# Performance work log

Measured on AMD Instinct MI355X. Metric: run time of the kernel, lower is better.

Reference implementation:

```python
import jax, jax.numpy as jnp
import numpy as np

D_MODEL = 768
D_COND = 128
N_LAYERS = 6
D_STATE = 16
D_CONV = 4
EXPAND = 2
D_INNER = EXPAND * D_MODEL            # 1536
DT_RANK = (D_MODEL + 15) // 16        # 48
BATCH, SEQ = 2, 1024
EPS = 1e-5


def setup_inputs() -> dict:
    key = jax.random.key(0)
    ks = iter(jax.random.split(key, 24))
    rn = lambda shape, s=0.02: jax.random.normal(next(ks), shape, dtype=jnp.float32) * s
    inp = {}
    inp["x"] = jax.random.normal(next(ks), (BATCH, SEQ, D_MODEL), dtype=jnp.float32)
    inp["condition"] = jax.random.normal(next(ks), (BATCH, D_COND), dtype=jnp.float32)
    # per-layer Mamba params, stacked on leading layer dim
    inp["in_proj_w"] = rn((N_LAYERS, 2 * D_INNER, D_MODEL))
    inp["conv_w"] = rn((N_LAYERS, D_INNER, D_CONV), 0.1)
    inp["conv_b"] = jnp.zeros((N_LAYERS, D_INNER), jnp.float32)
    inp["x_proj_w"] = rn((N_LAYERS, DT_RANK + 2 * D_STATE, D_INNER))
    inp["dt_proj_w"] = rn((N_LAYERS, D_INNER, DT_RANK), 0.1)
    inp["dt_proj_b"] = jnp.full((N_LAYERS, D_INNER), -4.0, jnp.float32)  # softplus -> small dt
    inp["A_log"] = jnp.tile(jnp.log(jnp.arange(1, D_STATE + 1, dtype=jnp.float32))[None, None, :], (N_LAYERS, D_INNER, 1))
    inp["D_skip"] = jnp.ones((N_LAYERS, D_INNER), jnp.float32)
    inp["out_proj_w"] = rn((N_LAYERS, D_MODEL, D_INNER))
    # post-residual LayerNorm affine per layer
    inp["norm_w"] = jnp.ones((N_LAYERS, D_MODEL), jnp.float32)
    inp["norm_b"] = jnp.zeros((N_LAYERS, D_MODEL), jnp.float32)
    # AdaLN: condition -> (scale, shift)
    inp["adaln_w"] = rn((N_LAYERS, 2 * D_MODEL, D_COND))
    inp["adaln_b"] = jnp.zeros((N_LAYERS, 2 * D_MODEL), jnp.float32)
    inp["final_norm_w"] = jnp.ones((D_MODEL,), jnp.float32)
    inp["final_norm_b"] = jnp.zeros((D_MODEL,), jnp.float32)
    return inp


def _ln(h, w, b):
    mu = jnp.mean(h, -1, keepdims=True)
    var = jnp.mean(jnp.square(h - mu), -1, keepdims=True)
    return (h - mu) * jax.lax.rsqrt(var + EPS) * w + b


def _ln_noaffine(h):
    mu = jnp.mean(h, -1, keepdims=True)
    var = jnp.mean(jnp.square(h - mu), -1, keepdims=True)
    return (h - mu) * jax.lax.rsqrt(var + EPS)


def _mamba(x, in_w, cw, cb, xp_w, dtp_w, dtp_b, A_log, D_skip, out_w):
    b, l, _ = x.shape
    xz = jnp.einsum('bld,ed->ble', x, in_w)                 # [b,l,2*di]
    xc, z = jnp.split(xz, 2, axis=-1)
    # causal depthwise conv over time
    xc_t = jnp.transpose(xc, (0, 2, 1))                     # [b,di,l]
    xc_t = jax.lax.conv_general_dilated(
        xc_t, cw[:, None, :], window_strides=(1,), padding=[(D_CONV - 1, 0)],
        dimension_numbers=('NCH', 'OIH', 'NCH'), feature_group_count=D_INNER)
    xc = jnp.transpose(xc_t + cb[None, :, None], (0, 2, 1))  # [b,l,di]
    xc = jax.nn.silu(xc)
    dbc = jnp.einsum('bld,ed->ble', xc, xp_w)                # [b,l,dt_rank+2*ds]
    dt = dbc[..., :DT_RANK]
    Bm = dbc[..., DT_RANK:DT_RANK + D_STATE]                 # [b,l,ds]
    Cm = dbc[..., DT_RANK + D_STATE:]                        # [b,l,ds]
    dt = jax.nn.softplus(jnp.einsum('blr,dr->bld', dt, dtp_w) + dtp_b)  # [b,l,di]
    A = -jnp.exp(A_log)                                      # [di,ds]

    def step(h, ts):
        dt_t, B_t, C_t, x_t = ts                             # [b,di],[b,ds],[b,ds],[b,di]
        dA = jnp.exp(dt_t[:, :, None] * A)                   # [b,di,ds]
        h = dA * h + (dt_t * x_t)[:, :, None] * B_t[:, None, :]
        y = jnp.sum(h * C_t[:, None, :], axis=-1)            # [b,di]
        return h, y

    h0 = jnp.zeros((b, D_INNER, D_STATE), x.dtype)
    ts = (jnp.transpose(dt, (1, 0, 2)), jnp.transpose(Bm, (1, 0, 2)),
          jnp.transpose(Cm, (1, 0, 2)), jnp.transpose(xc, (1, 0, 2)))
    h_final, y = jax.lax.scan(step, h0, ts)
    y = jnp.transpose(y, (1, 0, 2)) + D_skip * xc            # [b,l,di]
    y = y * jax.nn.silu(z)
    out = jnp.einsum('bld,ed->ble', y, out_w)                # [b,l,dm]
    return out, h_final


def reference(x, condition, in_proj_w, conv_w, conv_b, x_proj_w, dt_proj_w, dt_proj_b,
              A_log, D_skip, out_proj_w, norm_w, norm_b, adaln_w, adaln_b,
              final_norm_w, final_norm_b):
    h = x
    states = []
    for i in range(N_LAYERS):
        residual = h
        m, st = _mamba(h, in_proj_w[i], conv_w[i], conv_b[i], x_proj_w[i],
                       dt_proj_w[i], dt_proj_b[i], A_log[i], D_skip[i], out_proj_w[i])
        h = _ln(residual + m, norm_w[i], norm_b[i])
        ss = condition @ adaln_w[i].T + adaln_b[i]            # [b,2*dm]
        scale, shift = jnp.split(ss, 2, axis=-1)
        h = _ln_noaffine(h) * (1.0 + scale[:, None, :]) + shift[:, None, :]
        states.append(st)
    h = _ln(h, final_norm_w, final_norm_b)
    return h, jnp.stack(states)
```

## Files before the change

kernel.cpp:

```cpp
#include <hip/hip_runtime.h>
#include <hip/hip_bf16.h>

#define NL 6
#define DM 768
#define DI 1536
#define DS 16
#define NRANK 48
#define DBC 80
#define BATCH 2
#define SEQ 1024
#define NTOK (BATCH*SEQ)
#define NCHUNK 64
#define CHLEN 16
#define XKS 8
#define XKC (DI/XKS)

typedef __attribute__((ext_vector_type(8))) short short8;
typedef __attribute__((ext_vector_type(8))) unsigned short ushort8v;
typedef __attribute__((ext_vector_type(4))) float f32x4;
typedef __attribute__((ext_vector_type(4))) unsigned short ushort4v;

__device__ inline unsigned short f2bf(float f) {
  union { float f; unsigned u; } x; x.f = f;
  unsigned r = x.u + 0x7FFF + ((x.u >> 16) & 1);
  return (unsigned short)(r >> 16);
}
__device__ inline float bf2f(unsigned short s) {
  union { unsigned u; float f; } x; x.u = ((unsigned)s) << 16;
  return x.f;
}

__device__ inline void gl_lds16(const unsigned short* g, unsigned short* l) {
  __builtin_amdgcn_global_load_lds(
      (const __attribute__((address_space(1))) unsigned int*)(g),
      (__attribute__((address_space(3))) unsigned int*)(l),
      16, 0, 0);
}

#define V_X   (NTOK * DM / 8)
#define V_INW (NL * 2 * DI * DM / 8)
#define V_OUW (NL * DM * DI / 8)
#define V_XPW (NL * DBC * DI / 8)
#define V_DTW (NL * DI * 64 / 8)
#define V_NA  (NL * DI * DS / 8)
#define V_DTA (NTOK * 64 / 8)
#define V_ADA (NL * BATCH * 2 * DM)

__device__ inline ushort8v cvt8v(f32x4 a, f32x4 b) {
  union { ushort8v u8; __hip_bfloat162 h[4]; } u;
  float2 p;
  p.x = a[0]; p.y = a[1]; u.h[0] = __float22bfloat162_rn(p);
  p.x = a[2]; p.y = a[3]; u.h[1] = __float22bfloat162_rn(p);
  p.x = b[0]; p.y = b[1]; u.h[2] = __float22bfloat162_rn(p);
  p.x = b[2]; p.y = b[3]; u.h[3] = __float22bfloat162_rn(p);
  return u.u8;
}
__device__ inline void cvt8_store(const float* s, unsigned short* d, int i) {
  f32x4 a = ((const f32x4*)s)[i * 2];
  f32x4 b = ((const f32x4*)s)[i * 2 + 1];
  ((ushort8v*)d)[i] = cvt8v(a, b);
}

__global__ __launch_bounds__(256) void cvt_k(
    const float* __restrict__ x, const float* __restrict__ inw,
    const float* __restrict__ ouw, const float* __restrict__ xpw,
    const float* __restrict__ dtpw, const float* __restrict__ alog,
    const float* __restrict__ cond, const float* __restrict__ adaw,
    const float* __restrict__ adab,
    unsigned short* __restrict__ xb, unsigned short* __restrict__ inwb,
    unsigned short* __restrict__ ouwb, unsigned short* __restrict__ xpwb,
    unsigned short* __restrict__ dtwb, float* __restrict__ na,
    unsigned short* __restrict__ dtA, float* __restrict__ ss) {
  const int gid = blockIdx.x * 256 + threadIdx.x;
  const int stride = gridDim.x * 256;
  for (int i = gid; i < V_X; i += stride) cvt8_store(x, xb, i);
  for (int i = gid; i < V_INW; i += stride) cvt8_store(inw, inwb, i);
  for (int i = gid; i < V_OUW; i += stride) cvt8_store(ouw, ouwb, i);
  for (int i = gid; i < V_XPW; i += stride) cvt8_store(xpw, xpwb, i);
  for (int i = gid; i < V_DTW; i += stride) {
    int col8 = (i & 7) * 8;
    int row = i >> 3;
    ushort8v u8;
    if (col8 < NRANK) {
      const float* src = dtpw + (size_t)row * NRANK + col8;
      f32x4 a = *(const f32x4*)src;
      f32x4 b = *(const f32x4*)(src + 4);
      u8 = cvt8v(a, b);
    } else {
      u8 = (ushort8v){0,0,0,0,0,0,0,0};
    }
    *(ushort8v*)&dtwb[(size_t)row * 64 + col8] = u8;
  }
  for (int i = gid; i < V_NA; i += stride) {
    f32x4 a = ((const f32x4*)alog)[i * 2];
    f32x4 b = ((const f32x4*)alog)[i * 2 + 1];
    f32x4 ra, rb;
#pragma unroll
    for (int e = 0; e < 4; e++) { ra[e] = -__expf(a[e]); rb[e] = -__expf(b[e]); }
    ((f32x4*)na)[i * 2] = ra;
    ((f32x4*)na)[i * 2 + 1] = rb;
  }
  for (int i = gid; i < V_DTA; i += stride)
    ((ushort8v*)dtA)[i] = (ushort8v){0,0,0,0,0,0,0,0};
  for (int i = gid; i < V_ADA; i += stride) {
    int e = i % (2 * DM);
    int b = (i / (2 * DM)) % BATCH;
    int l = i / (BATCH * 2 * DM);
    const float* c = cond + b * 128;
    const float* wp = adaw + ((size_t)l * (2 * DM) + e) * 128;
    float s = adab[l * (2 * DM) + e];
    for (int kk = 0; kk < 128; kk++) s = fmaf(c[kk], wp[kk], s);
    ss[i] = s;
  }
}

__global__ __launch_bounds__(256) void bt128b_k(
    const unsigned short* __restrict__ A, int lda,
    const unsigned short* __restrict__ W, int ldw,
    unsigned short* __restrict__ C, int ldc,
    int K) {
  __shared__ __align__(16) unsigned short As[3][128 * 32];
  __shared__ __align__(16) unsigned short Ws[3][128 * 32];
  const int tid = threadIdx.x;
  const int bm = blockIdx.y * 128;
  const int bn = blockIdx.x * 128;
  const int lane = tid & 63;
  const int wv = tid >> 6;
  const int wm = (wv >> 1) * 64;
  const int wn = (wv & 1) * 64;
  const int fr = lane & 15;
  const int fs = lane >> 4;

  const int r0 = tid >> 2;
  const int s0 = (tid & 3) ^ (r0 & 3);

  const unsigned short* gA0 = A + (size_t)(bm + r0) * lda + s0 * 8;
  const unsigned short* gA1 = A + (size_t)(bm + r0 + 64) * lda + s0 * 8;
  const unsigned short* gW0 = W + (size_t)(bn + r0) * ldw + s0 * 8;
  const unsigned short* gW1 = W + (size_t)(bn + r0 + 64) * ldw + s0 * 8;

  f32x4 acc[4][4];
#pragma unroll
  for (int i = 0; i < 4; i++)
#pragma unroll
    for (int j = 0; j < 4; j++) acc[i][j] = (f32x4){0.f, 0.f, 0.f, 0.f};

  const int nk = K >> 5;
  gl_lds16(gA0, &As[0][0] + tid * 8);
  gl_lds16(gA1, &As[0][2048] + tid * 8);
  gl_lds16(gW0, &Ws[0][0] + tid * 8);
  gl_lds16(gW1, &Ws[0][2048] + tid * 8);
  if (nk > 1) {
    gl_lds16(gA0 + 32, &As[1][0] + tid * 8);
    gl_lds16(gA1 + 32, &As[1][2048] + tid * 8);
    gl_lds16(gW0 + 32, &Ws[1][0] + tid * 8);
    gl_lds16(gW1 + 32, &Ws[1][2048] + tid * 8);
  }

  for (int kk = 0; kk < nk; kk++) {
    const int b = kk % 3;
    if (kk + 2 < nk) {
      const int k0 = (kk + 2) * 32;
      const int nb = (kk + 2) % 3;
      gl_lds16(gA0 + k0, &As[nb][0] + tid * 8);
      gl_lds16(gA1 + k0, &As[nb][2048] + tid * 8);
      gl_lds16(gW0 + k0, &Ws[nb][0] + tid * 8);
      gl_lds16(gW1 + k0, &Ws[nb][2048] + tid * 8);
    }
    const int ahead = (nk - 1 - kk >= 2) ? 2 : (nk - 1 - kk);
    if (ahead == 2)      asm volatile("s_waitcnt vmcnt(8)" : : : "memory");
    else if (ahead == 1) asm volatile("s_waitcnt vmcnt(4)" : : : "memory");
    else                 asm volatile("s_waitcnt vmcnt(0)" : : : "memory");
    __builtin_amdgcn_s_barrier();
    __builtin_amdgcn_sched_barrier(0);

    short8 af[4], bf[4];
#pragma unroll
    for (int i = 0; i < 4; i++) {
      int rowa = wm + i * 16 + fr;
      af[i] = *(const short8*)&As[b][rowa * 32 + ((fs ^ (rowa & 3)) * 8)];
      int rowb = wn + i * 16 + fr;
      bf[i] = *(const short8*)&Ws[b][rowb * 32 + ((fs ^ (rowb & 3)) * 8)];
    }
#pragma unroll
    for (int i = 0; i < 4; i++)
#pragma unroll
      for (int j = 0; j < 4; j++)
        acc[i][j] = __builtin_amdgcn_mfma_f32_16x16x32_bf16(af[i], bf[j], acc[i][j], 0, 0, 0);

    __builtin_amdgcn_s_barrier();
  }

#pragma unroll
  for (int i = 0; i < 4; i++) {
#pragma unroll
    for (int j = 0; j < 4; j++) {
#pragma unroll
      for (int r = 0; r < 4; r++) {
        int row = bm + wm + i * 16 + fs * 4 + r;
        int col = bn + wn + j * 16 + fr;
        C[(size_t)row * ldc + col] = f2bf(acc[i][j][r]);
      }
    }
  }
}

template<int EPI>
__global__ __launch_bounds__(256) void bt64_k(
    const unsigned short* __restrict__ A, int lda,
    const unsigned short* __restrict__ W, int ldw,
    void* __restrict__ Cv, int ldc,
    int K,
    const float* __restrict__ bias) {
  __shared__ __align__(16) unsigned short As[3][64 * 32];
  __shared__ __align__(16) unsigned short Ws[3][64 * 32];
  const int tid = threadIdx.x;
  const int bm = blockIdx.y * 64;
  const int bn = blockIdx.x * 64;
  const int kz = (EPI == 3) ? blockIdx.z : 0;
  const int lane = tid & 63;
  const int wv = tid >> 6;
  const int wm = (wv >> 1) * 32;
  const int wn = (wv & 1) * 32;
  const int fr = lane & 15;
  const int fs = lane >> 4;

  const int r0 = tid >> 2;
  const int s0 = (tid & 3) ^ (r0 & 3);

  const unsigned short* gA = A + (size_t)(bm + r0) * lda + kz * K + s0 * 8;
  const unsigned short* gW = W + (size_t)(bn + r0) * ldw + kz * K + s0 * 8;

  f32x4 acc[2][2];
#pragma unroll
  for (int i = 0; i < 2; i++)
#pragma unroll
    for (int j = 0; j < 2; j++) acc[i][j] = (f32x4){0.f, 0.f, 0.f, 0.f};

  const int nk = K >> 5;
  gl_lds16(gA, &As[0][0] + tid * 8);
  gl_lds16(gW, &Ws[0][0] + tid * 8);
  if (nk > 1) {
    gl_lds16(gA + 32, &As[1][0] + tid * 8);
    gl_lds16(gW + 32, &Ws[1][0] + tid * 8);
  }

  for (int kk = 0; kk < nk; kk++) {
    const int b = kk % 3;
    if (kk + 2 < nk) {
      const int k0 = (kk + 2) * 32;
      const int nb = (kk + 2) % 3;
      gl_lds16(gA + k0, &As[nb][0] + tid * 8);
      gl_lds16(gW + k0, &Ws[nb][0] + tid * 8);
    }
    const int ahead = (nk - 1 - kk >= 2) ? 2 : (nk - 1 - kk);
    if (ahead == 2)      asm volatile("s_waitcnt vmcnt(4)" : : : "memory");
    else if (ahead == 1) asm volatile("s_waitcnt vmcnt(2)" : : : "memory");
    else                 asm volatile("s_waitcnt vmcnt(0)" : : : "memory");
    __builtin_amdgcn_s_barrier();
    __builtin_amdgcn_sched_barrier(0);

    short8 af[2], bf[2];
#pragma unroll
    for (int i = 0; i < 2; i++) {
      int rowa = wm + i * 16 + fr;
      af[i] = *(const short8*)&As[b][rowa * 32 + ((fs ^ (rowa & 3)) * 8)];
      int rowb = wn + i * 16 + fr;
      bf[i] = *(const short8*)&Ws[b][rowb * 32 + ((fs ^ (rowb & 3)) * 8)];
    }
#pragma unroll
    for (int i = 0; i < 2; i++)
#pragma unroll
      for (int j = 0; j < 2; j++)
        acc[i][j] = __builtin_amdgcn_mfma_f32_16x16x32_bf16(af[i], bf[j], acc[i][j], 0, 0, 0);

    __builtin_amdgcn_s_barrier();
  }

#pragma unroll
  for (int i = 0; i < 2; i++) {
#pragma unroll
    for (int j = 0; j < 2; j++) {
#pragma unroll
      for (int r = 0; r < 4; r++) {
        int row = bm + wm + i * 16 + fs * 4 + r;
        int col = bn + wn + j * 16 + fr;
        float v = acc[i][j][r];
        if (EPI == 1) {
          float xv = v + bias[col];
          float sp = (xv > 20.f) ? xv : log1pf(__expf(xv));
          ((unsigned short*)Cv)[(size_t)row * ldc + col] = f2bf(sp);
        }
        if (EPI == 3) {
          ((float*)Cv)[((size_t)kz * NTOK + row) * ldc + col] = v;
        }
      }
    }
  }
}

__global__ __launch_bounds__(256) void xp_k(
    const unsigned short* __restrict__ A,
    const unsigned short* __restrict__ W,
    unsigned short* __restrict__ part) {
  __shared__ __align__(16) unsigned short As[64][40];
  __shared__ __align__(16) unsigned short Ws[80][40];
  const int tid = threadIdx.x;
  const int ks = blockIdx.x;
  const int bm = blockIdx.y * 64;
  const int lane = tid & 63;
  const int wv = tid >> 6;
  const int fr = lane & 15;
  const int fs = lane >> 4;
  const int fk = fs * 8;

  const int ar = tid >> 2;
  const int ac = (tid & 3) * 8;
  const int k0base = ks * XKC;

  const unsigned short* gA  = A + (size_t)(bm + ar) * DI + k0base + ac;
  const unsigned short* gW0 = W + (size_t)ar * DI + k0base + ac;
  const unsigned short* gW1 = W + (size_t)(64 + ar) * DI + k0base + ac;

  f32x4 acc[5];
#pragma unroll
  for (int n = 0; n < 5; n++) acc[n] = (f32x4){0.f, 0.f, 0.f, 0.f};

  short8 aA, w0A, w1A;
  aA = *(const short8*)(gA);
  w0A = *(const short8*)(gW0);
  if (tid < 64) w1A = *(const short8*)(gW1);

  const int nk = XKC / 32;
  for (int kk = 0; kk < nk; kk++) {
    __syncthreads();
    *(short8*)&As[ar][ac] = aA;
    *(short8*)&Ws[ar][ac] = w0A;
    if (tid < 64) *(short8*)&Ws[64 + ar][ac] = w1A;
    __syncthreads();

    if (kk + 1 < nk) {
      const int k0 = (kk + 1) * 32;
      aA = *(const short8*)(gA + k0);
      w0A = *(const short8*)(gW0 + k0);
      if (tid < 64) w1A = *(const short8*)(gW1 + k0);
    }

    short8 af = *(const short8*)&As[wv * 16 + fr][fk];
#pragma unroll
    for (int n = 0; n < 5; n++) {
      short8 bf = *(const short8*)&Ws[n * 16 + fr][fk];
      acc[n] = __builtin_amdgcn_mfma_f32_16x16x32_bf16(af, bf, acc[n], 0, 0, 0);
    }
  }

#pragma unroll
  for (int n = 0; n < 5; n++) {
#pragma unroll
    for (int r = 0; r < 4; r++) {
      int row = bm + wv * 16 + fs * 4 + r;
      part[((size_t)ks * NTOK + row) * DBC + n * 16 + fr] = f2bf(acc[n][r]);
    }
  }
}

__global__ __launch_bounds__(256) void xp_reduce_k(const unsigned short* __restrict__ part,
                                                   unsigned short* __restrict__ dtA,
                                                   unsigned short* __restrict__ bc) {
  int i = blockIdx.x * 256 + threadIdx.x;
  const ushort4v* p4 = (const ushort4v*)part;
  const int stride4 = NTOK * DBC / 4;
  float s0 = 0.f, s1 = 0.f, s2 = 0.f, s3 = 0.f;
#pragma unroll
  for (int ks = 0; ks < XKS; ks++) {
    ushort4v v = p4[(size_t)ks * stride4 + i];
    s0 += bf2f(v[0]); s1 += bf2f(v[1]); s2 += bf2f(v[2]); s3 += bf2f(v[3]);
  }
  ushort4v o;
  o[0] = f2bf(s0); o[1] = f2bf(s1); o[2] = f2bf(s2); o[3] = f2bf(s3);
  int c4 = (i * 4) % DBC;
  int m = (i * 4) / DBC;
  if (c4 < NRANK) {
    *(ushort4v*)&dtA[(size_t)m * 64 + c4] = o;
  } else {
    *(ushort4v*)&bc[(size_t)m * 32 + (c4 - NRANK)] = o;
  }
}

__global__ __launch_bounds__(256) void conv_silu_k(const unsigned short* __restrict__ xz,
                                                   const float* __restrict__ cw,
                                                   const float* __restrict__ cb,
                                                   unsigned short* __restrict__ xcb) {
  const int d0 = (blockIdx.x * 256 + threadIdx.x) * 2;
  const int l0 = blockIdx.y * 16;
  const int b = blockIdx.z;
  const size_t mbase = (size_t)b * SEQ;
  const float wa0 = cw[d0 * 4 + 0], wa1 = cw[d0 * 4 + 1];
  const float wa2 = cw[d0 * 4 + 2], wa3 = cw[d0 * 4 + 3];
  const float wb0 = cw[d0 * 4 + 4], wb1 = cw[d0 * 4 + 5];
  const float wb2 = cw[d0 * 4 + 6], wb3 = cw[d0 * 4 + 7];
  const float ba = cb[d0], bb = cb[d0 + 1];

  float a3 = 0.f, a2 = 0.f, a1 = 0.f, b3 = 0.f, b2 = 0.f, b1 = 0.f;
  if (l0 >= 3) { ushort2 u = *(const ushort2*)&xz[(mbase + l0 - 3) * (2 * DI) + d0]; a3 = bf2f(u.x); b3 = bf2f(u.y); }
  if (l0 >= 2) { ushort2 u = *(const ushort2*)&xz[(mbase + l0 - 2) * (2 * DI) + d0]; a2 = bf2f(u.x); b2 = bf2f(u.y); }
  if (l0 >= 1) { ushort2 u = *(const ushort2*)&xz[(mbase + l0 - 1) * (2 * DI) + d0]; a1 = bf2f(u.x); b1 = bf2f(u.y); }
#pragma unroll
  for (int t = 0; t < 16; t++) {
    const int l = l0 + t;
    ushort2 u = *(const ushort2*)&xz[(mbase + l) * (2 * DI) + d0];
    float ca = bf2f(u.x), cbv = bf2f(u.y);
    float sa = ba + wa0 * a3 + wa1 * a2 + wa2 * a1 + wa3 * ca;
    float sb = bb + wb0 * b3 + wb1 * b2 + wb2 * b1 + wb3 * cbv;
    float ra = sa / (1.f + __expf(-sa));
    float rb = sb / (1.f + __expf(-sb));
    ushort2 o; o.x = f2bf(ra); o.y = f2bf(rb);
    *(ushort2*)&xcb[(mbase + l) * DI + d0] = o;
    a3 = a2; a2 = a1; a1 = ca;
    b3 = b2; b2 = b1; b1 = cbv;
  }
}

__global__ __launch_bounds__(256) void scan1_k(const unsigned short* __restrict__ dt,
                                               const unsigned short* __restrict__ xc,
                                               const unsigned short* __restrict__ bc,
                                               const float* __restrict__ negA_l,
                                               unsigned int* __restrict__ ch_pk,
                                               unsigned int* __restrict__ yc_pk) {
  __shared__ float Bs[CHLEN][DS];
  __shared__ float Cs[CHLEN][DS];
  const int tid = threadIdx.x;
  const int j = blockIdx.x;
  const int cg = blockIdx.y;
  const int b = cg / 6;
  const int d = (cg % 6) * 256 + tid;
  const int c = b * DI + d;
  const int m0 = b * SEQ + j * CHLEN;

  for (int e = tid; e < CHLEN * 32; e += 256) {
    int row = e >> 5, col = e & 31;
    float v = bf2f(bc[(size_t)(m0 + row) * 32 + col]);
    if (col < DS) Bs[row][col] = v; else Cs[row][col - DS] = v;
  }

  float Av[DS];
  const float* na = negA_l + (size_t)d * DS;
#pragma unroll
  for (int s = 0; s < DS; s++) Av[s] = na[s];
  const float Av0 = Av[0];
  bool fast = true;
#pragma unroll
  for (int s = 0; s < DS; s++)
    fast = fast && (fabsf(Av[s] - (s + 1) * Av0) <= 1e-4f * (s + 1));

  float dts[CHLEN], xcs[CHLEN];
#pragma unroll
  for (int t = 0; t < CHLEN; t++) {
    dts[t] = bf2f(dt[(size_t)(m0 + t) * DI + d]);
    xcs[t] = bf2f(xc[(size_t)(m0 + t) * DI + d]);
  }
  __syncthreads();

  float h[DS];
#pragma unroll
  for (int s = 0; s < DS; s++) h[s] = 0.f;
  float cd = 0.f;

  for (int t = 0; t < CHLEN; t++) {
    float dtv = dts[t];
    cd += dtv;
    float dtx = dtv * xcs[t];
    float ysum = 0.f;
    if (fast) {
      float e1 = __expf(dtv * Av0);
      float dA = e1;
      h[0] = fmaf(dA, h[0], dtx * Bs[t][0]);
      ysum = fmaf(h[0], Cs[t][0], ysum);
#pragma unroll
      for (int s = 1; s < DS; s++) {
        dA *= e1;
        h[s] = fmaf(dA, h[s], dtx * Bs[t][s]);
        ysum = fmaf(h[s], Cs[t][s], ysum);
      }
    } else {
#pragma unroll
      for (int s = 0; s < DS; s++) {
        float dA = __expf(dtv * Av[s]);
        h[s] = fmaf(dA, h[s], dtx * Bs[t][s]);
        ysum = fmaf(h[s], Cs[t][s], ysum);
      }
    }
    yc_pk[(size_t)(m0 + t) * DI + d] =
        (unsigned int)f2bf(ysum) | ((unsigned int)f2bf(cd) << 16);
  }

  size_t base = ((size_t)j * (BATCH * DI) + c) * DS;
#pragma unroll
  for (int s = 0; s < DS; s++) {
    unsigned int pk = (unsigned int)f2bf(__expf(cd * Av[s]))
                    | ((unsigned int)f2bf(h[s]) << 16);
    ch_pk[base + s] = pk;
  }
}

__global__ __launch_bounds__(256) void scan2_k(const unsigned int* __restrict__ ch_pk,
                                               unsigned short* __restrict__ hin,
                                               float* __restrict__ states_out) {
  int idx = blockIdx.x * 256 + threadIdx.x;
  const int stride = BATCH * DI * DS;
  float h = 0.f;
  for (int g = 0; g < NCHUNK / 8; g++) {
    unsigned int pks[8];
#pragma unroll
    for (int u = 0; u < 8; u++)
      pks[u] = ch_pk[(size_t)(g * 8 + u) * stride + idx];
#pragma unroll
    for (int u = 0; u < 8; u++) {
      hin[(size_t)(g * 8 + u) * stride + idx] = f2bf(h);
      h = fmaf(bf2f((unsigned short)(pks[u] & 0xFFFF)), h,
               bf2f((unsigned short)(pks[u] >> 16)));
    }
  }
  states_out[idx] = h;
}

__global__ __launch_bounds__(256) void scanfix_k(const unsigned int* __restrict__ yc_pk,
                                                 const unsigned short* __restrict__ xc,
                                                 const unsigned short* __restrict__ xz,
                                                 const unsigned short* __restrict__ bc,
                                                 const float* __restrict__ negA_l,
                                                 const float* __restrict__ Dsk,
                                                 const unsigned short* __restrict__ hin,
                                                 unsigned short* __restrict__ y) {
  int idx = blockIdx.x * 256 + threadIdx.x;
  int d = idx % DI;
  int m = idx / DI;
  int b = m / SEQ;
  int j = (m % SEQ) / CHLEN;
  unsigned int pk = yc_pk[idx];
  float yv = bf2f((unsigned short)(pk & 0xFFFF));
  float cd = bf2f((unsigned short)(pk >> 16));
  const f32x4* na4 = (const f32x4*)(negA_l + (size_t)d * DS);
  const ushort4v* cp4 = (const ushort4v*)(bc + (size_t)m * 32 + DS);
  const ushort4v* h4 = (const ushort4v*)(hin + ((size_t)j * (BATCH * DI) + (size_t)b * DI + d) * DS);
  float corr = 0.f;
#pragma unroll
  for (int q = 0; q < 4; q++) {
    f32x4 na = na4[q];
    ushort4v cp = cp4[q];
    ushort4v hh = h4[q];
#pragma unroll
    for (int e = 0; e < 4; e++)
      corr = fmaf(__expf(cd * na[e]) * bf2f(hh[e]), bf2f(cp[e]), corr);
  }
  yv += corr;
  float xv = bf2f(xc[idx]);
  float zv = bf2f(xz[(size_t)m * (2 * DI) + DI + d]);
  float sig = 1.f / (1.f + __expf(-zv));
  y[idx] = f2bf((yv + Dsk[d] * xv) * (zv * sig));
}

template<bool ADA>
__global__ __launch_bounds__(256) void ln_k(const float* __restrict__ in,
                                            const float* __restrict__ resid,
                                            const float* __restrict__ w,
                                            const float* __restrict__ bb,
                                            const float* __restrict__ ss,
                                            float* __restrict__ out,
                                            unsigned short* __restrict__ outb) {
  __shared__ float red[8];
  const int row = blockIdx.x;
  const int bt = row / SEQ;
  const int tid = threadIdx.x;
  float v[3];
#pragma unroll
  for (int i = 0; i < 3; i++) {
    int c = tid + i * 256;
    if (ADA) {
      v[i] = in[(size_t)row * DM + c] + in[(size_t)(NTOK + row) * DM + c]
           + resid[(size_t)row * DM + c];
    } else {
      v[i] = in[(size_t)row * DM + c];
    }
  }
  float s1 = v[0] + v[1] + v[2];
  float s2 = v[0]*v[0] + v[1]*v[1] + v[2]*v[2];
#pragma unroll
  for (int o = 32; o > 0; o >>= 1) { s1 += __shfl_down(s1, o); s2 += __shfl_down(s2, o); }
  int wv = tid >> 6, ln = tid & 63;
  if (ln == 0) { red[wv*2] = s1; red[wv*2+1] = s2; }
  __syncthreads();
  s1 = red[0] + red[2] + red[4] + red[6];
  s2 = red[1] + red[3] + red[5] + red[7];
  float mu = s1 * (1.f / DM);
  float var = s2 * (1.f / DM) - mu * mu;
  float rs = rsqrtf(var + 1e-5f);
  float t[3];
#pragma unroll
  for (int i = 0; i < 3; i++) {
    int c = tid + i * 256;
    t[i] = (v[i] - mu) * rs * w[c] + bb[c];
  }
  if (!ADA) {
#pragma unroll
    for (int i = 0; i < 3; i++) out[(size_t)row * DM + tid + i * 256] = t[i];
    return;
  }
  __syncthreads();
  s1 = t[0] + t[1] + t[2];
  s2 = t[0]*t[0] + t[1]*t[1] + t[2]*t[2];
#pragma unroll
  for (int o = 32; o > 0; o >>= 1) { s1 += __shfl_down(s1, o); s2 += __shfl_down(s2, o); }
  if (ln == 0) { red[wv*2] = s1; red[wv*2+1] = s2; }
  __syncthreads();
  s1 = red[0] + red[2] + red[4] + red[6];
  s2 = red[1] + red[3] + red[5] + red[7];
  float mu2 = s1 * (1.f / DM);
  float var2 = s2 * (1.f / DM) - mu2 * mu2;
  float rs2 = rsqrtf(var2 + 1e-5f);
#pragma unroll
  for (int i = 0; i < 3; i++) {
    int c = tid + i * 256;
    float sc = ss[bt * (2 * DM) + c];
    float sh = ss[bt * (2 * DM) + DM + c];
    float r = (t[i] - mu2) * rs2 * (1.f + sc) + sh;
    out[(size_t)row * DM + c] = r;
    outb[(size_t)row * DM + c] = f2bf(r);
  }
}

extern "C" void kernel_launch(void* const* d_in, const int* in_sizes, int n_in,
                              void* d_out, int out_size, void* d_ws, size_t ws_size,
                              hipStream_t stream) {
  const float* x      = (const float*)d_in[0];
  const float* cond   = (const float*)d_in[1];
  const float* in_w   = (const float*)d_in[2];
  const float* conv_w = (const float*)d_in[3];
  const float* conv_b = (const float*)d_in[4];
  const float* xp_w   = (const float*)d_in[5];
  const float* dtp_w  = (const float*)d_in[6];
  const float* dtp_b  = (const float*)d_in[7];
  const float* A_log  = (const float*)d_in[8];
  const float* Dsk    = (const float*)d_in[9];
  const float* out_w  = (const float*)d_in[10];
  const float* norm_w = (const float*)d_in[11];
  const float* norm_b = (const float*)d_in[12];
  const float* ada_w  = (const float*)d_in[13];
  const float* ada_b  = (const float*)d_in[14];
  const float* fn_w   = (const float*)d_in[15];
  const float* fn_b   = (const float*)d_in[16];

  float* out_h = (float*)d_out;
  float* out_states = out_h + (size_t)NTOK * DM;

  float* p = (float*)d_ws;
  float* h_cur = p; p += (size_t)NTOK * DM;
  float* part2 = p; p += (size_t)2 * NTOK * DM;
  float* ss    = p; p += (size_t)NL * BATCH * 2 * DM;
  float* negA  = p; p += (size_t)NL * DI * DS;
  unsigned int* ch_pk = (unsigned int*)p; p += (size_t)NCHUNK * BATCH * DI * DS;
  unsigned int* yc_pk = (unsigned int*)p; p += (size_t)NTOK * DI;
  unsigned short* q = (unsigned short*)p;
  unsigned short* hin      = q; q += (size_t)NCHUNK * BATCH * DI * DS;
  unsigned short* in_w_bf  = q; q += (size_t)NL * 2 * DI * DM;
  unsigned short* out_w_bf = q; q += (size_t)NL * DM * DI;
  unsigned short* xp_w_bf  = q; q += (size_t)NL * DBC * DI;
  unsigned short* dtw_bf   = q; q += (size_t)NL * DI * 64;
  unsigned short* h_bf     = q; q += (size_t)NTOK * DM;
  unsigned short* xz_bf    = q; q += (size_t)NTOK * 2 * DI;
  unsigned short* xc_bf    = q; q += (size_t)NTOK * DI;
  unsigned short* dtb_bf   = q; q += (size_t)NTOK * DI;
  unsigned short* yb_bf    = q; q += (size_t)NTOK * DI;
  unsigned short* part_bf  = q; q += (size_t)XKS * NTOK * DBC;
  unsigned short* dtA_bf   = q; q += (size_t)NTOK * 64;
  unsigned short* bc_bf    = q; q += (size_t)NTOK * 32;

  cvt_k<<<2048, 256, 0, stream>>>(x, in_w, out_w, xp_w, dtp_w, A_log,
                                  cond, ada_w, ada_b,
                                  h_bf, in_w_bf, out_w_bf, xp_w_bf, dtw_bf,
                                  negA, dtA_bf, ss);

  for (int l = 0; l < NL; l++) {
    bt128b_k<<<dim3(24, 16), 256, 0, stream>>>(
        h_bf, DM, in_w_bf + (size_t)l * 2 * DI * DM, DM, xz_bf, 2 * DI, DM);
    conv_silu_k<<<dim3(DI / 512, SEQ / 16, BATCH), 256, 0, stream>>>(
        xz_bf, conv_w + (size_t)l * DI * 4, conv_b + (size_t)l * DI, xc_bf);
    xp_k<<<dim3(XKS, NTOK / 64), 256, 0, stream>>>(
        xc_bf, xp_w_bf + (size_t)l * DBC * DI, part_bf);
    xp_reduce_k<<<NTOK * DBC / 4 / 256, 256, 0, stream>>>(part_bf, dtA_bf, bc_bf);
    bt64_k<1><<<dim3(DI / 64, NTOK / 64), 256, 0, stream>>>(
        dtA_bf, 64, dtw_bf + (size_t)l * DI * 64, 64, dtb_bf, DI,
        64, dtp_b + (size_t)l * DI);
    scan1_k<<<dim3(NCHUNK, 12), 256, 0, stream>>>(
        dtb_bf, xc_bf, bc_bf, negA + (size_t)l * DI * DS, ch_pk, yc_pk);
    scan2_k<<<192, 256, 0, stream>>>(
        ch_pk, hin, out_states + (size_t)l * BATCH * DI * DS);
    scanfix_k<<<NTOK * DI / 256, 256, 0, stream>>>(
        yc_pk, xc_bf, xz_bf, bc_bf, negA + (size_t)l * DI * DS,
        Dsk + (size_t)l * DI, hin, yb_bf);
    bt64_k<3><<<dim3(DM / 64, NTOK / 64, 2), 256, 0, stream>>>(
        yb_bf, DI, out_w_bf + (size_t)l * DM * DI, DI, part2, DM,
        DI / 2, nullptr);
    ln_k<true><<<NTOK, 256, 0, stream>>>(
        part2, (l == 0) ? x : h_cur,
        norm_w + (size_t)l * DM, norm_b + (size_t)l * DM,
        ss + (size_t)l * BATCH * 2 * DM, h_cur, h_bf);
  }
  ln_k<false><<<NTOK, 256, 0, stream>>>(h_cur, nullptr, fn_w, fn_b, nullptr,
                                        out_h, nullptr);
}
```

Before: 698.1 us.

## Fuse causal conv+SiLU into in_proj GEMM epilogue with boundary fixup kernel

The in_proj GEMM now stages its 128x128 output tile in shared memory and applies the depthwise causal conv and SiLU for the x half directly, writing xc. A small fixup kernel recomputes the first three rows of each 128-row tile, whose conv window reaches into the previous tile. This removes the separate conv kernel's re-read of xz, at the cost of extra epilogue work and a serial 61-64 step loop per thread. The fp32-to-bf16 conversion loops are also unrolled by two.

After: 722.6 us. +3.5%, slower.

```diff
diff --git a/kernel.cpp b/kernel.cpp
--- a/kernel.cpp
+++ b/kernel.cpp
@@ -73,10 +73,22 @@
     unsigned short* __restrict__ dtA, float* __restrict__ ss) {
   const int gid = blockIdx.x * 256 + threadIdx.x;
   const int stride = gridDim.x * 256;
-  for (int i = gid; i < V_X; i += stride) cvt8_store(x, xb, i);
-  for (int i = gid; i < V_INW; i += stride) cvt8_store(inw, inwb, i);
-  for (int i = gid; i < V_OUW; i += stride) cvt8_store(ouw, ouwb, i);
-  for (int i = gid; i < V_XPW; i += stride) cvt8_store(xpw, xpwb, i);
+  for (int i = gid; i < V_X / 2; i += stride) {
+    cvt8_store(x, xb, i);
+    cvt8_store(x, xb, i + V_X / 2);
+  }
+  for (int i = gid; i < V_INW / 2; i += stride) {
+    cvt8_store(inw, inwb, i);
+    cvt8_store(inw, inwb, i + V_INW / 2);
+  }
+  for (int i = gid; i < V_OUW / 2; i += stride) {
+    cvt8_store(ouw, ouwb, i);
+    cvt8_store(ouw, ouwb, i + V_OUW / 2);
+  }
+  for (int i = gid; i < V_XPW / 2; i += stride) {
+    cvt8_store(xpw, xpwb, i);
+    cvt8_store(xpw, xpwb, i + V_XPW / 2);
+  }
   for (int i = gid; i < V_DTW; i += stride) {
     int col8 = (i & 7) * 8;
     int row = i >> 3;
@@ -118,9 +130,13 @@
     const unsigned short* __restrict__ A, int lda,
     const unsigned short* __restrict__ W, int ldw,
     unsigned short* __restrict__ C, int ldc,
-    int K) {
-  __shared__ __align__(16) unsigned short As[3][128 * 32];
-  __shared__ __align__(16) unsigned short Ws[3][128 * 32];
+    int K,
+    const float* __restrict__ cw,
+    const float* __restrict__ cb,
+    unsigned short* __restrict__ xcb) {
+  __shared__ __align__(16) unsigned short SH[6 * 128 * 32];
+  unsigned short* Asp = SH;
+  unsigned short* Wsp = SH + 3 * 128 * 32;
   const int tid = threadIdx.x;
   const int bm = blockIdx.y * 128;
   const int bn = blockIdx.x * 128;
@@ -146,15 +162,15 @@
     for (int j = 0; j < 4; j++) acc[i][j] = (f32x4){0.f, 0.f, 0.f, 0.f};
 
   const int nk = K >> 5;
-  gl_lds16(gA0, &As[0][0] + tid * 8);
-  gl_lds16(gA1, &As[0][2048] + tid * 8);
-  gl_lds16(gW0, &Ws[0][0] + tid * 8);
-  gl_lds16(gW1, &Ws[0][2048] + tid * 8);
+  gl_lds16(gA0, Asp + tid * 8);
+  gl_lds16(gA1, Asp + 2048 + tid * 8);
+  gl_lds16(gW0, Wsp + tid * 8);
+  gl_lds16(gW1, Wsp + 2048 + tid * 8);
   if (nk > 1) {
-    gl_lds16(gA0 + 32, &As[1][0] + tid * 8);
-    gl_lds16(gA1 + 32, &As[1][2048] + tid * 8);
-    gl_lds16(gW0 + 32, &Ws[1][0] + tid * 8);
-    gl_lds16(gW1 + 32, &Ws[1][2048] + tid * 8);
+    gl_lds16(gA0 + 32, Asp + 4096 + tid * 8);
+    gl_lds16(gA1 + 32, Asp + 4096 + 2048 + tid * 8);
+    gl_lds16(gW0 + 32, Wsp + 4096 + tid * 8);
+    gl_lds16(gW1 + 32, Wsp + 4096 + 2048 + tid * 8);
   }
 
   for (int kk = 0; kk < nk; kk++) {
@@ -162,10 +178,10 @@
     if (kk + 2 < nk) {
       const int k0 = (kk + 2) * 32;
       const int nb = (kk + 2) % 3;
-      gl_lds16(gA0 + k0, &As[nb][0] + tid * 8);
-      gl_lds16(gA1 + k0, &As[nb][2048] + tid * 8);
-      gl_lds16(gW0 + k0, &Ws[nb][0] + tid * 8);
-      gl_lds16(gW1 + k0, &Ws[nb][2048] + tid * 8);
+      gl_lds16(gA0 + k0, Asp + nb * 4096 + tid * 8);
+      gl_lds16(gA1 + k0, Asp + nb * 4096 + 2048 + tid * 8);
+      gl_lds16(gW0 + k0, Wsp + nb * 4096 + tid * 8);
+      gl_lds16(gW1 + k0, Wsp + nb * 4096 + 2048 + tid * 8);
     }
     const int ahead = (nk - 1 - kk >= 2) ? 2 : (nk - 1 - kk);
     if (ahead == 2)      asm volatile("s_waitcnt vmcnt(8)" : : : "memory");
@@ -178,9 +194,9 @@
 #pragma unroll
     for (int i = 0; i < 4; i++) {
       int rowa = wm + i * 16 + fr;
-      af[i] = *(const short8*)&As[b][rowa * 32 + ((fs ^ (rowa & 3)) * 8)];
+      af[i] = *(const short8*)&Asp[b * 4096 + rowa * 32 + ((fs ^ (rowa & 3)) * 8)];
       int rowb = wn + i * 16 + fr;
-      bf[i] = *(const short8*)&Ws[b][rowb * 32 + ((fs ^ (rowb & 3)) * 8)];
+      bf[i] = *(const short8*)&Wsp[b * 4096 + rowb * 32 + ((fs ^ (rowb & 3)) * 8)];
     }
 #pragma unroll
     for (int i = 0; i < 4; i++)
@@ -203,6 +219,60 @@
       }
     }
   }
+
+  if (bn < DI) {
+    unsigned short* T = SH;
+    __syncthreads();
+#pragma unroll
+    for (int i = 0; i < 4; i++)
+#pragma unroll
+      for (int j = 0; j < 4; j++)
+#pragma unroll
+        for (int r = 0; r < 4; r++) {
+          int row = wm + i * 16 + fs * 4 + r;
+          int col = wn + j * 16 + fr;
+          T[row * 128 + col] = f2bf(acc[i][j][r]);
+        }
+    __syncthreads();
+
+    const int c = tid & 127;
+    const int half = tid >> 7;
+    const int d = bn + c;
+    const float w0 = cw[d * 4 + 0], w1 = cw[d * 4 + 1];
+    const float w2 = cw[d * 4 + 2], w3 = cw[d * 4 + 3];
+    const float bias = cb[d];
+    const int start = half ? 64 : 3;
+    const int end = half ? 128 : 64;
+    float c3 = bf2f(T[(start - 3) * 128 + c]);
+    float c2 = bf2f(T[(start - 2) * 128 + c]);
+    float c1 = bf2f(T[(start - 1) * 128 + c]);
+    for (int t = start; t < end; t++) {
+      float cur = bf2f(T[t * 128 + c]);
+      float s = bias + w0 * c3 + w1 * c2 + w2 * c1 + w3 * cur;
+      float sig = 1.f / (1.f + __expf(-s));
+      xcb[(size_t)(bm + t) * DI + d] = f2bf(s * sig);
+      c3 = c2; c2 = c1; c1 = cur;
+    }
+  }
+}
+
+__global__ __launch_bounds__(256) void convfix_k(const unsigned short* __restrict__ xz,
+                                                 const float* __restrict__ cw,
+                                                 const float* __restrict__ cb,
+                                                 unsigned short* __restrict__ xcb) {
+  int idx = blockIdx.x * 256 + threadIdx.x;
+  int d = idx % DI;
+  int k = idx / DI;
+  int m = (k / 3) * 128 + (k % 3);
+  int l = m % SEQ;
+  float s = cb[d];
+#pragma unroll
+  for (int j = 0; j < 4; j++) {
+    int tl = l - 3 + j;
+    if (tl >= 0) s += bf2f(xz[(size_t)(m - 3 + j) * (2 * DI) + d]) * cw[d * 4 + j];
+  }
+  float sig = 1.f / (1.f + __expf(-s));
+  xcb[(size_t)m * DI + d] = f2bf(s * sig);
 }
 
 template<int EPI>
@@ -384,40 +454,6 @@
     *(ushort4v*)&dtA[(size_t)m * 64 + c4] = o;
   } else {
     *(ushort4v*)&bc[(size_t)m * 32 + (c4 - NRANK)] = o;
-  }
-}
-
-__global__ __launch_bounds__(256) void conv_silu_k(const unsigned short* __restrict__ xz,
-                                                   const float* __restrict__ cw,
-                                                   const float* __restrict__ cb,
-                                                   unsigned short* __restrict__ xcb) {
-  const int d0 = (blockIdx.x * 256 + threadIdx.x) * 2;
-  const int l0 = blockIdx.y * 16;
-  const int b = blockIdx.z;
-  const size_t mbase = (size_t)b * SEQ;
-  const float wa0 = cw[d0 * 4 + 0], wa1 = cw[d0 * 4 + 1];
-  const float wa2 = cw[d0 * 4 + 2], wa3 = cw[d0 * 4 + 3];
-  const float wb0 = cw[d0 * 4 + 4], wb1 = cw[d0 * 4 + 5];
-  const float wb2 = cw[d0 * 4 + 6], wb3 = cw[d0 * 4 + 7];
-  const float ba = cb[d0], bb = cb[d0 + 1];
-
-  float a3 = 0.f, a2 = 0.f, a1 = 0.f, b3 = 0.f, b2 = 0.f, b1 = 0.f;
-  if (l0 >= 3) { ushort2 u = *(const ushort2*)&xz[(mbase + l0 - 3) * (2 * DI) + d0]; a3 = bf2f(u.x); b3 = bf2f(u.y); }
-  if (l0 >= 2) { ushort2 u = *(const ushort2*)&xz[(mbase + l0 - 2) * (2 * DI) + d0]; a2 = bf2f(u.x); b2 = bf2f(u.y); }
-  if (l0 >= 1) { ushort2 u = *(const ushort2*)&xz[(mbase + l0 - 1) * (2 * DI) + d0]; a1 = bf2f(u.x); b1 = bf2f(u.y); }
-#pragma unroll
-  for (int t = 0; t < 16; t++) {
-    const int l = l0 + t;
-    ushort2 u = *(const ushort2*)&xz[(mbase + l) * (2 * DI) + d0];
-    float ca = bf2f(u.x), cbv = bf2f(u.y);
-    float sa = ba + wa0 * a3 + wa1 * a2 + wa2 * a1 + wa3 * ca;
-    float sb = bb + wb0 * b3 + wb1 * b2 + wb2 * b1 + wb3 * cbv;
-    float ra = sa / (1.f + __expf(-sa));
-    float rb = sb / (1.f + __expf(-sb));
-    ushort2 o; o.x = f2bf(ra); o.y = f2bf(rb);
-    *(ushort2*)&xcb[(mbase + l) * DI + d0] = o;
-    a3 = a2; a2 = a1; a1 = ca;
-    b3 = b2; b2 = b1; b1 = cbv;
   }
 }
 
@@ -682,8 +718,9 @@
 
   for (int l = 0; l < NL; l++) {
     bt128b_k<<<dim3(24, 16), 256, 0, stream>>>(
-        h_bf, DM, in_w_bf + (size_t)l * 2 * DI * DM, DM, xz_bf, 2 * DI, DM);
-    conv_silu_k<<<dim3(DI / 512, SEQ / 16, BATCH), 256, 0, stream>>>(
+        h_bf, DM, in_w_bf + (size_t)l * 2 * DI * DM, DM, xz_bf, 2 * DI, DM,
+        conv_w + (size_t)l * DI * 4, conv_b + (size_t)l * DI, xc_bf);
+    convfix_k<<<48 * DI / 256, 256, 0, stream>>>(
         xz_bf, conv_w + (size_t)l * DI * 4, conv_b + (size_t)l * DI, xc_bf);
     xp_k<<<dim3(XKS, NTOK / 64), 256, 0, stream>>>(
         xc_bf, xp_w_bf + (size_t)l * DBC * DI, part_bf);
```
